# Optimization experiments

Hardware: AMD Instinct MI355X
Metric: run time of the kernel (lower is better)

The kernel has to match this reference:

```python
import jax, jax.numpy as jnp
import numpy as np
from jax import lax

B, CIN, H, W = 8, 3, 256, 256
CMID = 16          # conv out channels == config.in_channels
DM = 256           # d_model
P = 2              # patch size (hardcoded in Downsample)
DI = 512           # d_inner = expand * d_model
NH, HD, NS, KC = 8, 64, 128, 4   # heads, headdim, d_state, d_conv
CONVDIM = DI + 2 * NS            # 768
PROJ = 2 * DI + 2 * NS + NH      # 1288


def _sincos2d(dim, gs):
    # 2d sin-cos positional embedding, matches get_2d_sincos_pos_embed
    def emb1d(d, pos):
        omega = 1.0 / (10000.0 ** (jnp.arange(d // 2, dtype=jnp.float32) / (d / 2.0)))
        out = pos[:, None] * omega[None, :]
        return jnp.concatenate([jnp.sin(out), jnp.cos(out)], axis=1)
    g = jnp.arange(gs, dtype=jnp.float32)
    grid = jnp.stack(jnp.meshgrid(g, g), 0).reshape(2, -1)  # [2, gs*gs]
    return jnp.concatenate([emb1d(dim // 2, grid[0]), emb1d(dim // 2, grid[1])], 1)


def _mamba2(u, in_proj_w, conv1d_w, conv1d_b, dt_bias, A_log, D, norm_w, out_proj_w):
    b, l, _ = u.shape
    zxbcdt = jnp.einsum('bld,pd->blp', u, in_proj_w)              # [b,l,1288]
    z = zxbcdt[..., :DI]
    xBC = zxbcdt[..., DI:DI + CONVDIM]
    dt = zxbcdt[..., DI + CONVDIM:]                                # [b,l,NH]
    # causal depthwise conv1d over sequence, then SiLU
    xc = lax.conv_general_dilated(xBC.transpose(0, 2, 1), conv1d_w, (1,), [(KC - 1, 0)],
                                  feature_group_count=CONVDIM,
                                  dimension_numbers=('NCH', 'OIH', 'NCH'))
    xBC = jax.nn.silu(xc + conv1d_b[None, :, None]).transpose(0, 2, 1)
    xh = xBC[..., :DI].reshape(b, l, NH, HD)                       # [b,l,h,p]
    Bm = xBC[..., DI:DI + NS]                                      # [b,l,n]
    Cm = xBC[..., DI + NS:]                                        # [b,l,n]
    dt = jax.nn.softplus(dt + dt_bias)                             # [b,l,h]
    dA = jnp.exp(dt * (-jnp.exp(A_log)))                           # [b,l,h]
    dtx = dt[..., None] * xh                                       # [b,l,h,p]

    def step(s, inp):
        dtx_t, B_t, C_t, dA_t = inp
        s = s * dA_t[..., None, None] + dtx_t[..., None] * B_t[:, None, None, :]
        return s, jnp.einsum('bhpn,bn->bhp', s, C_t)

    s0 = jnp.zeros((b, NH, HD, NS), u.dtype)
    _, ys = lax.scan(step, s0, (dtx.transpose(1, 0, 2, 3), Bm.transpose(1, 0, 2),
                                Cm.transpose(1, 0, 2), dA.transpose(1, 0, 2)))
    y = ys.transpose(1, 0, 2, 3) + D[None, None, :, None] * xh     # [b,l,h,p]
    y = y.reshape(b, l, DI) * jax.nn.silu(z)                       # gated
    y = y * lax.rsqrt(jnp.mean(y * y, -1, keepdims=True) + 1e-5) * norm_w
    return jnp.einsum('bld,od->blo', y, out_proj_w)


def setup_inputs() -> dict:
    key = jax.random.key(0)
    ks = jax.random.split(key, 12)
    r = lambda i, s, sc: jax.random.normal(ks[i], s, jnp.float32) * sc
    return {
        'x': jax.random.normal(ks[0], (B, CIN, H, W), jnp.float32),
        'conv_w': r(1, (CMID, CIN, 3, 3), 0.1), 'conv_b': jnp.zeros((CMID,), jnp.float32),
        'bn_gamma': jnp.ones((CMID,), jnp.float32), 'bn_beta': jnp.zeros((CMID,), jnp.float32),
        'patch_w': r(2, (DM, CMID, P, P), 0.1), 'patch_b': jnp.zeros((DM,), jnp.float32),
        'in_proj_w': r(3, (PROJ, DM), 0.02),
        'conv1d_w': r(4, (CONVDIM, 1, KC), 0.1), 'conv1d_b': jnp.zeros((CONVDIM,), jnp.float32),
        'dt_bias': r(5, (NH,), 0.5),
        'A_log': jax.random.uniform(ks[6], (NH,), jnp.float32),
        'D': jnp.ones((NH,), jnp.float32),
        'norm_w': jnp.ones((DI,), jnp.float32),
        'out_proj_w': r(7, (DM, DI), 0.02),
        'final_w': r(8, (P * P * CMID, DM), 0.02), 'final_b': jnp.zeros((P * P * CMID,), jnp.float32),
    }


def reference(x, conv_w, conv_b, bn_gamma, bn_beta, patch_w, patch_b, in_proj_w,
              conv1d_w, conv1d_b, dt_bias, A_log, D, norm_w, out_proj_w, final_w, final_b):
    # Conv2d k=3 s=2 p=1 -> BatchNorm2d (training-mode batch stats) -> GELU
    h = lax.conv_general_dilated(x, conv_w, (2, 2), [(1, 1), (1, 1)],
                                 dimension_numbers=('NCHW', 'OIHW', 'NCHW')) + conv_b[None, :, None, None]
    mu = jnp.mean(h, (0, 2, 3), keepdims=True)
    var = jnp.var(h, (0, 2, 3), keepdims=True)
    h = (h - mu) * lax.rsqrt(var + 1e-5) * bn_gamma[None, :, None, None] + bn_beta[None, :, None, None]
    h = jax.nn.gelu(h, approximate=False)
    # PatchEmbed: conv k=p s=p, flatten to tokens, add frozen sincos pos embed
    t = lax.conv_general_dilated(h, patch_w, (P, P), 'VALID',
                                 dimension_numbers=('NCHW', 'OIHW', 'NCHW')) + patch_b[None, :, None, None]
    b, d, gh, gw = t.shape
    tok = t.reshape(b, d, gh * gw).transpose(0, 2, 1) + _sincos2d(DM, gh)[None]
    # MambaBlock: Mamba2(x) + x  (layers=1; repo loop discards all but last layer)
    y = _mamba2(tok, in_proj_w, conv1d_w, conv1d_b, dt_bias, A_log, D, norm_w, out_proj_w) + tok
    # FinalLayer: linear only (norm_final is unused in its forward)
    o = jnp.einsum('bld,od->blo', y, final_w) + final_b
    # unpatchify
    o = o.reshape(b, gh, gw, P, P, CMID)
    o = jnp.einsum('nhwpqc->nchpwq', o).reshape(b, CMID, gh * P, gw * P)
    return o
```

## Files before the change

kernel.cpp:

```cpp
#include <hip/hip_runtime.h>
#include <math.h>

#define B_  8
#define CIN 3
#define HIN 256
#define WIN 256
#define CMID 16
#define HMID 128
#define WMID 128
#define DM 256
#define L_ 4096
#define DI 512
#define NH 8
#define HD 64
#define NS 128
#define KC 4
#define CONVDIM 768
#define PROJ 1288
#define NPADIN 1408
#define MTOK (B_*L_)
#define QCH 128
#define NCH 32

typedef unsigned short bf16;
typedef __attribute__((ext_vector_type(8))) short bf16x8;
typedef __attribute__((ext_vector_type(4))) float f32x4;

__device__ inline float bf2f(bf16 u) { return __uint_as_float(((unsigned int)u) << 16); }
__device__ inline bf16 f2bf(float f) {
  unsigned int x = __float_as_uint(f);
  return (bf16)((x + 0x7fffu + ((x >> 16) & 1u)) >> 16);
}
__device__ inline unsigned int pack2bf(float a, float b) {
  return (unsigned int)f2bf(a) | ((unsigned int)f2bf(b) << 16);
}

__global__ void k_conv1(const float* __restrict__ x, const float* __restrict__ w,
                        const float* __restrict__ bias, float* __restrict__ out) {
  int idx = blockIdx.x*256 + threadIdx.x;
  if (idx >= B_*CMID*HMID*WMID) return;
  int xo = idx & 127, yo = (idx>>7)&127, co = (idx>>14)&15, b = idx>>18;
  float acc = bias[co];
  const float* xb = x + (size_t)b*CIN*HIN*WIN;
  const float* wc = w + co*CIN*9;
  #pragma unroll
  for (int ci=0; ci<CIN; ci++)
    #pragma unroll
    for (int ky=0; ky<3; ky++) {
      int yi = 2*yo - 1 + ky;
      if (yi < 0 || yi >= HIN) continue;
      #pragma unroll
      for (int kx=0; kx<3; kx++) {
        int xi = 2*xo - 1 + kx;
        if (xi < 0 || xi >= WIN) continue;
        acc += xb[(ci*HIN + yi)*WIN + xi] * wc[(ci*3+ky)*3+kx];
      }
    }
  out[idx] = acc;
}

__global__ __launch_bounds__(256) void k_bnstatsA(const float* __restrict__ h, float2* __restrict__ part) {
  int blk = blockIdx.x;
  const float4* base = (const float4*)(h + ((size_t)(blk>>2))*16384 + (blk&3)*4096);
  int tid = threadIdx.x;
  float s=0.f, s2=0.f;
  #pragma unroll
  for (int i=0;i<4;i++){
    float4 v = base[i*256 + tid];
    s += v.x+v.y+v.z+v.w;
    s2 += v.x*v.x + v.y*v.y + v.z*v.z + v.w*v.w;
  }
  #pragma unroll
  for (int off=1; off<64; off<<=1) { s += __shfl_xor(s, off); s2 += __shfl_xor(s2, off); }
  __shared__ float sb[2][4];
  if ((tid&63)==0){ sb[0][tid>>6]=s; sb[1][tid>>6]=s2; }
  __syncthreads();
  if (tid==0) part[blk] = make_float2(sb[0][0]+sb[0][1]+sb[0][2]+sb[0][3],
                                      sb[1][0]+sb[1][1]+sb[1][2]+sb[1][3]);
}

__global__ void k_bnstatsB(const float2* __restrict__ part, float* __restrict__ stats) {
  int lane = threadIdx.x;
  int c = lane >> 2, j0 = lane & 3;
  float s=0.f, s2=0.f;
  #pragma unroll
  for (int j=j0; j<32; j+=4){
    int b = j >> 2, chunk = j & 3;
    float2 p = part[(b*16+c)*4 + chunk];
    s += p.x; s2 += p.y;
  }
  s += __shfl_xor(s,1); s2 += __shfl_xor(s2,1);
  s += __shfl_xor(s,2); s2 += __shfl_xor(s2,2);
  if (j0==0){
    const float inv = 1.f/131072.f;
    float mean = s*inv;
    float var  = s2*inv - mean*mean;
    stats[c]      = mean;
    stats[16 + c] = rsqrtf(var + 1e-5f);
  }
}

__global__ __launch_bounds__(256) void k_patch(const float* __restrict__ h, const float* __restrict__ pw,
                       const float* __restrict__ pb, const float* __restrict__ stats,
                       const float* __restrict__ gamma, const float* __restrict__ beta,
                       bf16* __restrict__ tok) {
  int grp = blockIdx.x;
  int b = grp >> 9, g8 = grp & 511;
  int g0 = g8 << 3;
  int gy = g0 >> 6, gx0 = g0 & 63;
  __shared__ float sh[8][64];
  int tid = threadIdx.x;
  {
    int tk = tid >> 5, jj = (tid & 31)*2;
    int ci = jj >> 2, p = (jj >> 1) & 1;
    const float* src = &h[((size_t)(b*CMID+ci)*HMID + 2*gy+p)*WMID + 2*(gx0+tk)];
    float2 xv = *(const float2*)src;
    float mean = stats[ci], rstd = stats[16+ci];
    float sc = rstd*gamma[ci], be = beta[ci] - mean*sc;
    float v0 = xv.x*sc + be;
    float v1 = xv.y*sc + be;
    v0 = 0.5f*v0*(1.f + erff(v0*0.70710678118654752f));
    v1 = 0.5f*v1*(1.f + erff(v1*0.70710678118654752f));
    sh[tk][jj] = v0; sh[tk][jj+1] = v1;
  }
  __syncthreads();
  int d = tid;
  float wr[64];
  #pragma unroll
  for (int i4=0;i4<16;i4++) *(float4*)&wr[i4*4] = *(const float4*)&pw[d*64 + i4*4];
  float bias = pb[d];
  int i = d & 63;
  float omega = expf(-(float)i * (9.210340371976184f/64.f));
  #pragma unroll
  for (int tk=0;tk<8;tk++){
    float acc = bias;
    #pragma unroll
    for (int j=0;j<64;j++) acc = fmaf(sh[tk][j], wr[j], acc);
    float gv = (d < 128) ? (float)(gx0+tk) : (float)gy;
    float ph = gv * omega;
    float pos = (d & 64) ? __cosf(ph) : __sinf(ph);
    tok[((size_t)((b<<12) + g0 + tk))*DM + d] = f2bf(acc + pos);
  }
}

__global__ void k_cvtw(const float* __restrict__ src, bf16* __restrict__ dst,
                       int N, int kshift, int total) {
  int idx = blockIdx.x*256 + threadIdx.x;
  if (idx >= total) return;
  int n = idx >> kshift;
  dst[idx] = (n < N) ? f2bf(src[idx]) : (bf16)0;
}

template<int EPI>
__global__ __launch_bounds__(256) void k_mgemm(
    const bf16* __restrict__ A, const bf16* __restrict__ Bw, int K,
    bf16* __restrict__ o_z, bf16* __restrict__ o_x,
    bf16* __restrict__ o_y, const bf16* __restrict__ res,
    const float* __restrict__ dt_bias, const float* __restrict__ A_log,
    float* __restrict__ dtv, float* __restrict__ dAv,
    float* __restrict__ o_f, const float* __restrict__ fbias) {
  __shared__ __align__(16) bf16 sA[2][128*32];
  __shared__ __align__(16) bf16 sB[2][128*32];
  int tid = threadIdx.x;
  int lane = tid & 63, wid = tid >> 6;
  int wr = wid >> 1, wc = wid & 1;
  int m0 = blockIdx.x*128, n0 = blockIdx.y*128;
  int nk = K >> 5;
  f32x4 acc[4][4];
  #pragma unroll
  for (int i=0;i<4;i++)
    #pragma unroll
    for (int j=0;j<4;j++)
      acc[i][j] = (f32x4){0.f,0.f,0.f,0.f};

  auto stage = [&](int buf, int ks){
    int kk = ks << 5;
    #pragma unroll
    for (int i=0;i<2;i++){
      int j = i*256 + tid;
      int row = j >> 2, cc = j & 3;
      int kg = cc ^ (row & 3);
      unsigned ldsoff = (unsigned)((i*256 + wid*64) * 16);
      __builtin_amdgcn_global_load_lds(
        (const __attribute__((address_space(1))) void*)(A + (size_t)(m0+row)*K + kk + kg*8),
        (__attribute__((address_space(3))) void*)((char*)&sA[buf][0] + ldsoff), 16, 0, 0);
      __builtin_amdgcn_global_load_lds(
        (const __attribute__((address_space(1))) void*)(Bw + (size_t)(n0+row)*K + kk + kg*8),
        (__attribute__((address_space(3))) void*)((char*)&sB[buf][0] + ldsoff), 16, 0, 0);
    }
  };

  int r = lane & 15, q = lane >> 4;
  int kgo = (q ^ (r & 3)) << 3;

  stage(0, 0);
  for (int ks=0; ks<nk; ++ks){
    int cur = ks & 1;
    __syncthreads();
    if (ks+1 < nk) stage(cur^1, ks+1);
    bf16x8 af[4], bfv[4];
    #pragma unroll
    for (int mf=0;mf<4;mf++){
      int rowm = wr*64 + mf*16 + r;
      af[mf] = *(const bf16x8*)&sA[cur][rowm*32 + kgo];
    }
    #pragma unroll
    for (int nf=0;nf<4;nf++){
      int rown = wc*64 + nf*16 + r;
      bfv[nf] = *(const bf16x8*)&sB[cur][rown*32 + kgo];
    }
    #pragma unroll
    for (int mf=0;mf<4;mf++)
      #pragma unroll
      for (int nf=0;nf<4;nf++)
        acc[mf][nf] = __builtin_amdgcn_mfma_f32_16x16x32_bf16(af[mf], bfv[nf], acc[mf][nf], 0, 0, 0);
  }

  #pragma unroll
  for (int mf=0;mf<4;mf++){
    #pragma unroll
    for (int nf=0;nf<4;nf++){
      int n = n0 + wc*64 + nf*16 + r;
      int mbase = m0 + wr*64 + mf*16 + q*4;
      #pragma unroll
      for (int rr=0;rr<4;rr++){
        int m = mbase + rr;
        float val = acc[mf][nf][rr];
        if (EPI == 0){
          if (n < DI) {
            o_z[(size_t)m*DI + n] = f2bf(val);
          } else if (n < DI + CONVDIM) {
            o_x[(size_t)m*CONVDIM + (n - DI)] = f2bf(val);
          } else if (n < PROJ) {
            int hh = n - (DI + CONVDIM);
            float xv = val + dt_bias[hh];
            float dt = (xv > 20.f) ? xv : log1pf(expf(xv));
            dtv[(size_t)m*NH + hh] = dt;
            dAv[(size_t)m*NH + hh] = expf(-expf(A_log[hh]) * dt);
          }
        } else if (EPI == 1) {
          o_y[(size_t)m*DM + n] = f2bf(val + bf2f(res[(size_t)m*DM + n]));
        } else {
          if (n < 64) {
            float vv = val + fbias[n];
            int b = m >> 12, g = m & 4095;
            int gy = g >> 6, gx = g & 63;
            int p = n >> 5, qq = (n>>4)&1, cc2 = n & 15;
            o_f[(((size_t)(b*CMID+cc2))*HMID + 2*gy+p)*WMID + (2*gx+qq)] = vv;
          }
        }
      }
    }
  }
}

__global__ __launch_bounds__(256) void k_conv1d(const bf16* __restrict__ xpre, const float* __restrict__ cw,
                         const float* __restrict__ cb, bf16* __restrict__ xbc) {
  int idx = blockIdx.x*256 + threadIdx.x;
  int gch = idx % 96;
  int tb  = idx / 96;
  int ch0 = gch*8;
  int bl0 = tb*8;
  int l0 = bl0 & (L_-1);
  float wv[32];
  #pragma unroll
  for (int i=0;i<8;i++) *(float4*)&wv[i*4] = *(const float4*)&cw[ch0*KC + i*4];
  float bs[8];
  *(float4*)&bs[0] = *(const float4*)&cb[ch0];
  *(float4*)&bs[4] = *(const float4*)&cb[ch0+4];
  uint4 rows[11];
  #pragma unroll
  for (int j=0;j<11;j++){
    int lk = l0 - 3 + j;
    if (lk < 0) rows[j] = make_uint4(0u,0u,0u,0u);
    else rows[j] = *(const uint4*)(xpre + ((size_t)bl0 - 3 + j)*CONVDIM + ch0);
  }
  #pragma unroll
  for (int t=0;t<8;t++){
    float acc[8];
    #pragma unroll
    for (int i=0;i<8;i++) acc[i] = bs[i];
    #pragma unroll
    for (int k=0;k<KC;k++){
      uint4 u = rows[t+k];
      unsigned uu[4]={u.x,u.y,u.z,u.w};
      #pragma unroll
      for (int c2=0;c2<4;c2++){
        float lo = __uint_as_float(uu[c2]<<16);
        float hi = __uint_as_float(uu[c2]&0xffff0000u);
        acc[c2*2]   = fmaf(wv[(c2*2)*4 + k],   lo, acc[c2*2]);
        acc[c2*2+1] = fmaf(wv[(c2*2+1)*4 + k], hi, acc[c2*2+1]);
      }
    }
    unsigned ou[4];
    #pragma unroll
    for (int c2=0;c2<4;c2++){
      float v0 = acc[c2*2], v1 = acc[c2*2+1];
      v0 = v0 / (1.f + __expf(-v0));
      v1 = v1 / (1.f + __expf(-v1));
      ou[c2] = pack2bf(v0, v1);
    }
    *(uint4*)(xbc + (size_t)(bl0+t)*CONVDIM + ch0) = make_uint4(ou[0],ou[1],ou[2],ou[3]);
  }
}

__global__ __launch_bounds__(256) void k_ssd1(const bf16* __restrict__ xbc,
    const float* __restrict__ dtv, const float* __restrict__ A_log,
    bf16* __restrict__ ys, bf16* __restrict__ Sst) {
  int blk = blockIdx.x;
  int c = blk & (NCH-1), h = (blk>>5)&7, b = blk>>8;
  int tid = threadIdx.x;
  int lane = tid & 63, wid = tid >> 6;
  int r = lane & 15, q = lane >> 4;
  size_t rowbase = (size_t)b*L_ + (size_t)c*QCH;
  float eA = __expf(A_log[h]);

  __shared__ __align__(16) bf16 sB[128*128];
  __shared__ __align__(16) bf16 sC[128*128];
  __shared__ __align__(16) bf16 sDX[64*128];
  __shared__ __align__(16) bf16 sBT[128*128];
  __shared__ float sDT[128];
  __shared__ float sL[128];
  __shared__ float sWS[128];
  __shared__ float sWT[2];

  #pragma unroll
  for (int i=0;i<16;i++){
    int id = i*256 + tid;
    int row = id >> 5, cg = id & 31;
    uint4 u = *(const uint4*)(xbc + (rowbase+row)*CONVDIM + DI + cg*8);
    if (cg < 16) *(uint4*)&sB[row*128 + ((cg ^ (row&15))<<3)] = u;
    else { int cg2 = cg-16; *(uint4*)&sC[row*128 + ((cg2 ^ (row&15))<<3)] = u; }
  }
  if (tid < 128) sDT[tid] = dtv[(rowbase+tid)*NH + h];
  __syncthreads();

  float inc = 0.f;
  if (tid < 128){
    inc = sDT[tid];
    #pragma unroll
    for (int off=1; off<64; off<<=1){
      float u = __shfl_up(inc, off);
      if (lane >= off) inc += u;
    }
    if (lane==63) sWT[wid] = inc;
  }
  __syncthreads();
  if (tid < 128){
    if (wid==1) inc += sWT[0];
    sL[tid] = inc;
  }
  {
    int s = tid >> 1, ph = tid & 1;
    float dts = sDT[s];
    const bf16* xs = xbc + (rowbase+s)*CONVDIM + h*HD + ph*32;
    #pragma unroll
    for (int i8=0;i8<4;i8++){
      ushort4 u0 = *(const ushort4*)(xs + i8*8);
      ushort4 u1 = *(const ushort4*)(xs + i8*8 + 4);
      unsigned short uu[8] = {u0.x,u0.y,u0.z,u0.w,u1.x,u1.y,u1.z,u1.w};
      #pragma unroll
      for (int j=0;j<8;j++){
        int p = ph*32 + i8*8 + j;
        sDX[p*128 + (((s>>3) ^ (p&15))<<3) + (s&7)] = f2bf(dts * bf2f(uu[j]));
      }
    }
  }
  __syncthreads();

  int wr = wid >> 1, wc = wid & 1;
  f32x4 accG[4][4];
  #pragma unroll
  for (int i=0;i<4;i++)
    #pragma unroll
    for (int j=0;j<4;j++) accG[i][j] = (f32x4){0.f,0.f,0.f,0.f};
  #pragma unroll
  for (int ks=0; ks<4; ks++){
    bf16x8 af[4], bfv[4];
    #pragma unroll
    for (int mf=0;mf<4;mf++){
      int t = wr*64 + mf*16 + r;
      af[mf] = *(const bf16x8*)&sC[t*128 + (((ks*4+q) ^ (t&15))<<3)];
    }
    #pragma unroll
    for (int nf=0;nf<4;nf++){
      int s = wc*64 + nf*16 + r;
      bfv[nf] = *(const bf16x8*)&sB[s*128 + (((ks*4+q) ^ (s&15))<<3)];
    }
    #pragma unroll
    for (int mf=0;mf<4;mf++)
      #pragma unroll
      for (int nf=0;nf<4;nf++)
        accG[mf][nf] = __builtin_amdgcn_mfma_f32_16x16x32_bf16(af[mf], bfv[nf], accG[mf][nf], 0, 0, 0);
  }
  __syncthreads();

  bf16* sW = sC;
  #pragma unroll
  for (int mf=0;mf<4;mf++){
    #pragma unroll
    for (int nf=0;nf<4;nf++){
      int s = wc*64 + nf*16 + r;
      float Ls = sL[s];
      #pragma unroll
      for (int rr=0;rr<4;rr++){
        int t = wr*64 + mf*16 + q*4 + rr;
        float wvv = 0.f;
        if (s <= t) wvv = accG[mf][nf][rr] * __expf(-eA*(sL[t]-Ls));
        sW[t*128 + (((s>>3) ^ (t&15))<<3) + (s&7)] = f2bf(wvv);
      }
    }
  }
  if (tid < 128) sWS[tid] = __expf(-eA*(sL[127]-sL[tid]));
  __syncthreads();

  {
    int n = tid >> 1, ph = tid & 1;
    #pragma unroll
    for (int i8=0;i8<8;i8++){
      unsigned short vals[8];
      #pragma unroll
      for (int j=0;j<8;j++){
        int s = ph*64 + i8*8 + j;
        float bv = bf2f(sB[s*128 + (((n>>3) ^ (s&15))<<3) + (n&7)]);
        vals[j] = f2bf(bv * sWS[s]);
      }
      int s8 = ph*8 + i8;
      *(uint4*)&sBT[n*128 + ((s8 ^ (n&15))<<3)] = *(const uint4*)vals;
    }
  }
  __syncthreads();

  {
    int wr2 = wid >> 1, wc2 = wid & 1;
    f32x4 accY[4][2];
    #pragma unroll
    for (int i=0;i<4;i++){ accY[i][0]=(f32x4){0.f,0.f,0.f,0.f}; accY[i][1]=(f32x4){0.f,0.f,0.f,0.f}; }
    #pragma unroll
    for (int ks=0; ks<4; ks++){
      bf16x8 af[4], bfv[2];
      #pragma unroll
      for (int mf=0;mf<4;mf++){
        int t = wr2*64 + mf*16 + r;
        af[mf] = *(const bf16x8*)&sW[t*128 + (((ks*4+q) ^ (t&15))<<3)];
      }
      #pragma unroll
      for (int nf=0;nf<2;nf++){
        int p = wc2*32 + nf*16 + r;
        bfv[nf] = *(const bf16x8*)&sDX[p*128 + (((ks*4+q) ^ (p&15))<<3)];
      }
      #pragma unroll
      for (int mf=0;mf<4;mf++)
        #pragma unroll
        for (int nf=0;nf<2;nf++)
          accY[mf][nf] = __builtin_amdgcn_mfma_f32_16x16x32_bf16(af[mf], bfv[nf], accY[mf][nf], 0, 0, 0);
    }
    #pragma unroll
    for (int mf=0;mf<4;mf++){
      #pragma unroll
      for (int nf=0;nf<2;nf++){
        int p = wc2*32 + nf*16 + r;
        #pragma unroll
        for (int rr=0;rr<4;rr++){
          int t = wr2*64 + mf*16 + q*4 + rr;
          ys[(rowbase+t)*DI + h*HD + p] = f2bf(accY[mf][nf][rr]);
        }
      }
    }
  }

  {
    int wrp = wid >> 1, wcn = wid & 1;
    f32x4 accT[2][4];
    #pragma unroll
    for (int i=0;i<2;i++)
      #pragma unroll
      for (int j=0;j<4;j++) accT[i][j] = (f32x4){0.f,0.f,0.f,0.f};
    #pragma unroll
    for (int ks=0; ks<4; ks++){
      bf16x8 af[2], bfv[4];
      #pragma unroll
      for (int mf=0;mf<2;mf++){
        int p = wrp*32 + mf*16 + r;
        af[mf] = *(const bf16x8*)&sDX[p*128 + (((ks*4+q) ^ (p&15))<<3)];
      }
      #pragma unroll
      for (int nf=0;nf<4;nf++){
        int n = wcn*64 + nf*16 + r;
        bfv[nf] = *(const bf16x8*)&sBT[n*128 + (((ks*4+q) ^ (n&15))<<3)];
      }
      #pragma unroll
      for (int mf=0;mf<2;mf++)
        #pragma unroll
        for (int nf=0;nf<4;nf++)
          accT[mf][nf] = __builtin_amdgcn_mfma_f32_16x16x32_bf16(af[mf], bfv[nf], accT[mf][nf], 0, 0, 0);
    }
    size_t sb = (((size_t)(b*NH+h))*NCH + c)*8192;
    #pragma unroll
    for (int mf=0;mf<2;mf++){
      #pragma unroll
      for (int nf=0;nf<4;nf++){
        int n = wcn*64 + nf*16 + r;
        #pragma unroll
        for (int rr=0;rr<4;rr++){
          int p = wrp*32 + mf*16 + q*4 + rr;
          Sst[sb + (size_t)p*128 + n] = f2bf(accT[mf][nf][rr]);
        }
      }
    }
  }
}

template<int NCHT, int QCHT>
__global__ __launch_bounds__(256) void k_scan2(bf16* __restrict__ Sst, const float* __restrict__ dAv) {
  constexpr int SEG = QCHT/16;
  int blk = blockIdx.x;
  int bh = blk>>2, q = blk&3;
  int b = bh>>3, h = bh&7;
  int tid = threadIdx.x;
  __shared__ float sP[NCHT];
  {
    int c = tid / SEG, seg = tid & (SEG-1);
    float prod = 1.f;
    size_t base = ((size_t)b*L_ + c*QCHT + seg*16)*NH + h;
    #pragma unroll
    for (int k=0;k<16;k++) prod *= dAv[base + (size_t)k*NH];
    #pragma unroll
    for (int off=1; off<SEG; off<<=1) prod *= __shfl_xor(prod, off);
    if (seg==0) sP[c] = prod;
  }
  __syncthreads();
  int e0 = q*2048 + tid*8;
  float acc[8];
  #pragma unroll
  for (int j=0;j<8;j++) acc[j]=0.f;
  size_t sbase = (size_t)bh*NCHT*8192 + e0;
  for (int c=0;c<NCHT;c++){
    bf16* ptr = Sst + sbase + (size_t)c*8192;
    uint4 u = *(const uint4*)ptr;
    unsigned int uu[4] = {u.x,u.y,u.z,u.w};
    float tv[8];
    #pragma unroll
    for (int k=0;k<4;k++){
      tv[2*k]   = __uint_as_float(uu[k]<<16);
      tv[2*k+1] = __uint_as_float(uu[k]&0xffff0000u);
    }
    uint4 o;
    o.x = pack2bf(acc[0],acc[1]); o.y = pack2bf(acc[2],acc[3]);
    o.z = pack2bf(acc[4],acc[5]); o.w = pack2bf(acc[6],acc[7]);
    asm volatile("s_waitcnt vmcnt(0)" ::: "memory");
    *(uint4*)ptr = o;
    float P = sP[c];
    #pragma unroll
    for (int j=0;j<8;j++) acc[j] = tv[j] + P*acc[j];
  }
}

__global__ __launch_bounds__(256) void k_ssd3(const bf16* __restrict__ xbc,
    const float* __restrict__ dtv, const float* __restrict__ A_log,
    const bf16* __restrict__ Sst, bf16* __restrict__ ys) {
  int blk = blockIdx.x;
  int c = blk & (NCH-1), h = (blk>>5)&7, b = blk>>8;
  int tid = threadIdx.x;
  int lane = tid & 63, wid = tid >> 6;
  int r = lane & 15, q = lane >> 4;
  size_t rowbase = (size_t)b*L_ + (size_t)c*QCH;
  float eA = __expf(A_log[h]);

  __shared__ __align__(16) bf16 sC[128*128];
  __shared__ float sDT[128];
  __shared__ float sL[128];
  __shared__ float sAt[128];
  __shared__ float sWT[2];

  #pragma unroll
  for (int i=0;i<8;i++){
    int id = i*256 + tid;
    int row = id >> 4, cg = id & 15;
    uint4 u = *(const uint4*)(xbc + (rowbase+row)*CONVDIM + DI + NS + cg*8);
    *(uint4*)&sC[row*128 + ((cg ^ (row&15))<<3)] = u;
  }
  if (tid < 128) sDT[tid] = dtv[(rowbase+tid)*NH + h];
  __syncthreads();
  float inc = 0.f;
  if (tid < 128){
    inc = sDT[tid];
    #pragma unroll
    for (int off=1; off<64; off<<=1){
      float u = __shfl_up(inc, off);
      if (lane >= off) inc += u;
    }
    if (lane==63) sWT[wid] = inc;
  }
  __syncthreads();
  if (tid < 128){
    if (wid==1) inc += sWT[0];
    sL[tid] = inc;
    sAt[tid] = __expf(-eA*inc);
  }
  __syncthreads();

  int wr2 = wid >> 1, wc2 = wid & 1;
  size_t sb = (((size_t)(b*NH+h))*NCH + c)*8192;
  f32x4 accP[4][2];
  #pragma unroll
  for (int i=0;i<4;i++){ accP[i][0]=(f32x4){0.f,0.f,0.f,0.f}; accP[i][1]=(f32x4){0.f,0.f,0.f,0.f}; }
  #pragma unroll
  for (int ks=0; ks<4; ks++){
    bf16x8 af[4], bfv[2];
    #pragma unroll
    for (int mf=0;mf<4;mf++){
      int t = wr2*64 + mf*16 + r;
      af[mf] = *(const bf16x8*)&sC[t*128 + (((ks*4+q) ^ (t&15))<<3)];
    }
    #pragma unroll
    for (int nf=0;nf<2;nf++){
      int p = wc2*32 + nf*16 + r;
      bfv[nf] = *(const bf16x8*)(Sst + sb + (size_t)p*128 + ks*32 + q*8);
    }
    #pragma unroll
    for (int mf=0;mf<4;mf++)
      #pragma unroll
      for (int nf=0;nf<2;nf++)
        accP[mf][nf] = __builtin_amdgcn_mfma_f32_16x16x32_bf16(af[mf], bfv[nf], accP[mf][nf], 0, 0, 0);
  }
  #pragma unroll
  for (int mf=0;mf<4;mf++){
    #pragma unroll
    for (int nf=0;nf<2;nf++){
      int p = wc2*32 + nf*16 + r;
      #pragma unroll
      for (int rr=0;rr<4;rr++){
        int t = wr2*64 + mf*16 + q*4 + rr;
        bf16* yp = ys + (rowbase+t)*DI + h*HD + p;
        *yp = f2bf(bf2f(*yp) + sAt[t]*accP[mf][nf][rr]);
      }
    }
  }
}

__global__ __launch_bounds__(256) void k_combine(bf16* __restrict__ ys, const bf16* __restrict__ xbc,
                         const bf16* __restrict__ z, const float* __restrict__ Dp,
                         const float* __restrict__ nw) {
  int bl = blockIdx.x;
  int tid = threadIdx.x;
  bf16* yrow = ys + (size_t)bl*DI;
  const bf16* xrow = xbc + (size_t)bl*CONVDIM;
  const bf16* zrow = z + (size_t)bl*DI;
  float v[2]; float ss = 0.f;
  #pragma unroll
  for (int i=0;i<2;i++) {
    int d = tid + i*256;
    float xh = bf2f(xrow[d]);
    float y = bf2f(yrow[d]) + Dp[d>>6]*xh;
    float zv = bf2f(zrow[d]);
    y *= zv / (1.f + expf(-zv));
    v[i] = y; ss += y*y;
  }
  #pragma unroll
  for (int off=1; off<64; off<<=1) ss += __shfl_xor(ss, off);
  __shared__ float sb[4];
  if ((tid&63)==0) sb[tid>>6]=ss;
  __syncthreads();
  float total = sb[0]+sb[1]+sb[2]+sb[3];
  float scale = rsqrtf(total * (1.f/512.f) + 1e-5f);
  #pragma unroll
  for (int i=0;i<2;i++) {
    int d = tid + i*256;
    yrow[d] = f2bf(v[i]*scale*nw[d]);
  }
}

extern "C" void kernel_launch(void* const* d_in, const int* in_sizes, int n_in,
                              void* d_out, int out_size, void* d_ws, size_t ws_size,
                              hipStream_t stream) {
  const float* x         = (const float*)d_in[0];
  const float* conv_w    = (const float*)d_in[1];
  const float* conv_b    = (const float*)d_in[2];
  const float* bn_gamma  = (const float*)d_in[3];
  const float* bn_beta   = (const float*)d_in[4];
  const float* patch_w   = (const float*)d_in[5];
  const float* patch_b   = (const float*)d_in[6];
  const float* in_proj_w = (const float*)d_in[7];
  const float* conv1d_w  = (const float*)d_in[8];
  const float* conv1d_b  = (const float*)d_in[9];
  const float* dt_bias   = (const float*)d_in[10];
  const float* A_log     = (const float*)d_in[11];
  const float* Dp        = (const float*)d_in[12];
  const float* norm_w    = (const float*)d_in[13];
  const float* out_proj_w= (const float*)d_in[14];
  const float* final_w   = (const float*)d_in[15];
  const float* final_b   = (const float*)d_in[16];
  float* out = (float*)d_out;

  char* Wb = (char*)d_ws;
  float* h_buf = (float*)(Wb + 0);
  bf16*  winb  = (bf16*)(Wb + 0);
  bf16*  woutb = (bf16*)(Wb + 0);
  bf16*  wfinb = (bf16*)(Wb + 262144);
  bf16*  xpost = (bf16*)(Wb + 0);
  float2* part = (float2*)(Wb + 50331648);
  bf16*  tok   = (bf16*)(Wb + 50331648);
  bf16*  zbuf  = (bf16*)(Wb + 67108864);
  bf16*  y2b   = (bf16*)(Wb + 67108864);
  bf16*  xpre  = (bf16*)(Wb + 100663296);
  bf16*  ysb   = (bf16*)(Wb + 100663296);
  bf16*  Sst   = (bf16*)(Wb + 134217728);
  float* dtv   = (float*)(Wb + 134217728 + 33554432);
  float* dAv   = dtv + 262144;
  float* stats = dAv + 262144;
  const size_t NEED = 134217728ull + 33554432 + 2097152 + 256;
  if (ws_size < NEED) {
    hipMemsetAsync(d_out, 0, (size_t)out_size*sizeof(float), stream);
    return;
  }

  k_conv1<<<dim3((B_*CMID*HMID*WMID)/256), dim3(256), 0, stream>>>(x, conv_w, conv_b, h_buf);
  k_bnstatsA<<<dim3(512), dim3(256), 0, stream>>>(h_buf, part);
  k_bnstatsB<<<dim3(1), dim3(64), 0, stream>>>(part, stats);
  k_patch<<<dim3(MTOK/8), dim3(256), 0, stream>>>(h_buf, patch_w, patch_b, stats, bn_gamma, bn_beta, tok);
  k_cvtw<<<dim3((NPADIN*DM)/256), dim3(256), 0, stream>>>(in_proj_w, winb, PROJ, 8, NPADIN*DM);
  k_mgemm<0><<<dim3(MTOK/128, NPADIN/128), dim3(256), 0, stream>>>(tok, winb, DM,
      zbuf, xpre, nullptr, nullptr, dt_bias, A_log, dtv, dAv, nullptr, nullptr);
  k_conv1d<<<dim3((MTOK/8*96)/256), dim3(256), 0, stream>>>(xpre, conv1d_w, conv1d_b, xpost);
  k_ssd1<<<dim3(B_*NH*NCH), dim3(256), 0, stream>>>(xpost, dtv, A_log, ysb, Sst);
  k_scan2<NCH,QCH><<<dim3(B_*NH*4), dim3(256), 0, stream>>>(Sst, dAv);
  k_ssd3<<<dim3(B_*NH*NCH), dim3(256), 0, stream>>>(xpost, dtv, A_log, Sst, ysb);
  k_combine<<<dim3(MTOK), dim3(256), 0, stream>>>(ysb, xpost, zbuf, Dp, norm_w);
  k_cvtw<<<dim3((DM*DI)/256), dim3(256), 0, stream>>>(out_proj_w, woutb, DM, 9, DM*DI);
  k_cvtw<<<dim3((128*DM)/256), dim3(256), 0, stream>>>(final_w, wfinb, 64, 8, 128*DM);
  k_mgemm<1><<<dim3(MTOK/128, DM/128), dim3(256), 0, stream>>>(ysb, woutb, DI,
      nullptr, nullptr, y2b, tok, nullptr, nullptr, nullptr, nullptr, nullptr, nullptr);
  k_mgemm<2><<<dim3(MTOK/128, 1), dim3(256), 0, stream>>>(y2b, wfinb, DM,
      nullptr, nullptr, nullptr, nullptr, nullptr, nullptr, nullptr, nullptr, out, final_b);
}
```

Baseline: 383.8 us.

## Restructure SSD chunk kernel to 512 threads with transposed MFMA tiles and vector stores

k_ssd1 now runs 512 threads per block. Each GEMM is re-tiled so results land with contiguous output dimensions, which lets the ys and state stores be packed uint2 writes instead of scalar bf16 stores. The dt scaling moves out of the x staging into the decay weights (W and the B-transpose), so x is loaded raw with 16-byte loads and one barrier goes away. k_ssd3 is transposed in the same way to get vectorized read-modify-write of ys. The cost is more threads per block competing for the same large shared-memory footprint, and a changed rounding point for dt, since it is now applied in the weights rather than on x before the bf16 conversion.

Result: faster. 363.4 us (-5.3%).

```diff
diff --git a/kernel.cpp b/kernel.cpp
--- a/kernel.cpp
+++ b/kernel.cpp
@@ -304,7 +304,7 @@
   }
 }
 
-__global__ __launch_bounds__(256) void k_ssd1(const bf16* __restrict__ xbc,
+__global__ __launch_bounds__(512) void k_ssd1(const bf16* __restrict__ xbc,
     const float* __restrict__ dtv, const float* __restrict__ A_log,
     bf16* __restrict__ ys, bf16* __restrict__ Sst) {
   int blk = blockIdx.x;
@@ -325,13 +325,31 @@
   __shared__ float sWT[2];
 
   #pragma unroll
-  for (int i=0;i<16;i++){
-    int id = i*256 + tid;
+  for (int i=0;i<8;i++){
+    int id = i*512 + tid;
     int row = id >> 5, cg = id & 31;
     uint4 u = *(const uint4*)(xbc + (rowbase+row)*CONVDIM + DI + cg*8);
     if (cg < 16) *(uint4*)&sB[row*128 + ((cg ^ (row&15))<<3)] = u;
     else { int cg2 = cg-16; *(uint4*)&sC[row*128 + ((cg2 ^ (row&15))<<3)] = u; }
   }
+  {
+    int s0 = (tid >> 3)*2;
+    int p0 = (tid & 7)*8;
+    const bf16* x0 = xbc + (rowbase+s0)*CONVDIM + h*HD + p0;
+    uint4 u0 = *(const uint4*)x0;
+    uint4 u1 = *(const uint4*)(x0 + CONVDIM);
+    unsigned a0[4]={u0.x,u0.y,u0.z,u0.w}, a1[4]={u1.x,u1.y,u1.z,u1.w};
+    int cb2 = s0 >> 3, se = s0 & 7;
+    #pragma unroll
+    for (int jp=0;jp<4;jp++){
+      unsigned w0=a0[jp], w1=a1[jp];
+      unsigned lo = (w0 & 0xffffu) | (w1 << 16);
+      unsigned hi = (w0 >> 16) | (w1 & 0xffff0000u);
+      int pA = p0 + jp*2, pB = pA+1;
+      *(unsigned*)&sDX[pA*128 + ((cb2 ^ (pA&15))<<3) + se] = lo;
+      *(unsigned*)&sDX[pB*128 + ((cb2 ^ (pB&15))<<3) + se] = hi;
+    }
+  }
   if (tid < 128) sDT[tid] = dtv[(rowbase+tid)*NH + h];
   __syncthreads();
 
@@ -350,45 +368,28 @@
     if (wid==1) inc += sWT[0];
     sL[tid] = inc;
   }
-  {
-    int s = tid >> 1, ph = tid & 1;
-    float dts = sDT[s];
-    const bf16* xs = xbc + (rowbase+s)*CONVDIM + h*HD + ph*32;
-    #pragma unroll
-    for (int i8=0;i8<4;i8++){
-      ushort4 u0 = *(const ushort4*)(xs + i8*8);
-      ushort4 u1 = *(const ushort4*)(xs + i8*8 + 4);
-      unsigned short uu[8] = {u0.x,u0.y,u0.z,u0.w,u1.x,u1.y,u1.z,u1.w};
-      #pragma unroll
-      for (int j=0;j<8;j++){
-        int p = ph*32 + i8*8 + j;
-        sDX[p*128 + (((s>>3) ^ (p&15))<<3) + (s&7)] = f2bf(dts * bf2f(uu[j]));
-      }
-    }
-  }
-  __syncthreads();
 
   int wr = wid >> 1, wc = wid & 1;
-  f32x4 accG[4][4];
-  #pragma unroll
-  for (int i=0;i<4;i++)
+  f32x4 accG[2][4];
+  #pragma unroll
+  for (int i=0;i<2;i++)
     #pragma unroll
     for (int j=0;j<4;j++) accG[i][j] = (f32x4){0.f,0.f,0.f,0.f};
   #pragma unroll
   for (int ks=0; ks<4; ks++){
-    bf16x8 af[4], bfv[4];
-    #pragma unroll
-    for (int mf=0;mf<4;mf++){
-      int t = wr*64 + mf*16 + r;
-      af[mf] = *(const bf16x8*)&sC[t*128 + (((ks*4+q) ^ (t&15))<<3)];
+    bf16x8 af[2], bfv[4];
+    #pragma unroll
+    for (int mf=0;mf<2;mf++){
+      int s = wr*32 + mf*16 + r;
+      af[mf] = *(const bf16x8*)&sB[s*128 + (((ks*4+q) ^ (s&15))<<3)];
     }
     #pragma unroll
     for (int nf=0;nf<4;nf++){
-      int s = wc*64 + nf*16 + r;
-      bfv[nf] = *(const bf16x8*)&sB[s*128 + (((ks*4+q) ^ (s&15))<<3)];
-    }
-    #pragma unroll
-    for (int mf=0;mf<4;mf++)
+      int t = wc*64 + nf*16 + r;
+      bfv[nf] = *(const bf16x8*)&sC[t*128 + (((ks*4+q) ^ (t&15))<<3)];
+    }
+    #pragma unroll
+    for (int mf=0;mf<2;mf++)
       #pragma unroll
       for (int nf=0;nf<4;nf++)
         accG[mf][nf] = __builtin_amdgcn_mfma_f32_16x16x32_bf16(af[mf], bfv[nf], accG[mf][nf], 0, 0, 0);
@@ -397,115 +398,116 @@
 
   bf16* sW = sC;
   #pragma unroll
-  for (int mf=0;mf<4;mf++){
+  for (int mf=0;mf<2;mf++){
+    int sb4 = wr*32 + mf*16 + q*4;
+    int cb4 = sb4 >> 3, se4 = sb4 & 7;
     #pragma unroll
     for (int nf=0;nf<4;nf++){
-      int s = wc*64 + nf*16 + r;
-      float Ls = sL[s];
+      int t = wc*64 + nf*16 + r;
+      float Lt = sL[t];
+      float w[4];
       #pragma unroll
       for (int rr=0;rr<4;rr++){
-        int t = wr*64 + mf*16 + q*4 + rr;
-        float wvv = 0.f;
-        if (s <= t) wvv = accG[mf][nf][rr] * __expf(-eA*(sL[t]-Ls));
-        sW[t*128 + (((s>>3) ^ (t&15))<<3) + (s&7)] = f2bf(wvv);
-      }
-    }
-  }
-  if (tid < 128) sWS[tid] = __expf(-eA*(sL[127]-sL[tid]));
+        int s = sb4 + rr;
+        float v = 0.f;
+        if (s <= t) v = accG[mf][nf][rr] * sDT[s] * __expf(-eA*(Lt - sL[s]));
+        w[rr] = v;
+      }
+      *(uint2*)&sW[t*128 + ((cb4 ^ (t&15))<<3) + se4] =
+          make_uint2(pack2bf(w[0],w[1]), pack2bf(w[2],w[3]));
+    }
+  }
+  if (tid < 128) sWS[tid] = sDT[tid]*__expf(-eA*(sL[127]-sL[tid]));
   __syncthreads();
 
   {
-    int n = tid >> 1, ph = tid & 1;
-    #pragma unroll
-    for (int i8=0;i8<8;i8++){
+    int n = tid >> 2, sg = tid & 3;
+    #pragma unroll
+    for (int i8=0;i8<4;i8++){
       unsigned short vals[8];
       #pragma unroll
       for (int j=0;j<8;j++){
-        int s = ph*64 + i8*8 + j;
+        int s = sg*32 + i8*8 + j;
         float bv = bf2f(sB[s*128 + (((n>>3) ^ (s&15))<<3) + (n&7)]);
         vals[j] = f2bf(bv * sWS[s]);
       }
-      int s8 = ph*8 + i8;
+      int s8 = sg*4 + i8;
       *(uint4*)&sBT[n*128 + ((s8 ^ (n&15))<<3)] = *(const uint4*)vals;
     }
   }
   __syncthreads();
 
   {
-    int wr2 = wid >> 1, wc2 = wid & 1;
-    f32x4 accY[4][2];
-    #pragma unroll
-    for (int i=0;i<4;i++){ accY[i][0]=(f32x4){0.f,0.f,0.f,0.f}; accY[i][1]=(f32x4){0.f,0.f,0.f,0.f}; }
+    int wrp = wid >> 2, wct = wid & 3;
+    f32x4 acc2[2][2];
+    #pragma unroll
+    for (int i=0;i<2;i++){ acc2[i][0]=(f32x4){0.f,0.f,0.f,0.f}; acc2[i][1]=(f32x4){0.f,0.f,0.f,0.f}; }
     #pragma unroll
     for (int ks=0; ks<4; ks++){
-      bf16x8 af[4], bfv[2];
-      #pragma unroll
-      for (int mf=0;mf<4;mf++){
-        int t = wr2*64 + mf*16 + r;
-        af[mf] = *(const bf16x8*)&sW[t*128 + (((ks*4+q) ^ (t&15))<<3)];
-      }
-      #pragma unroll
-      for (int nf=0;nf<2;nf++){
-        int p = wc2*32 + nf*16 + r;
-        bfv[nf] = *(const bf16x8*)&sDX[p*128 + (((ks*4+q) ^ (p&15))<<3)];
-      }
-      #pragma unroll
-      for (int mf=0;mf<4;mf++)
-        #pragma unroll
-        for (int nf=0;nf<2;nf++)
-          accY[mf][nf] = __builtin_amdgcn_mfma_f32_16x16x32_bf16(af[mf], bfv[nf], accY[mf][nf], 0, 0, 0);
-    }
-    #pragma unroll
-    for (int mf=0;mf<4;mf++){
-      #pragma unroll
-      for (int nf=0;nf<2;nf++){
-        int p = wc2*32 + nf*16 + r;
-        #pragma unroll
-        for (int rr=0;rr<4;rr++){
-          int t = wr2*64 + mf*16 + q*4 + rr;
-          ys[(rowbase+t)*DI + h*HD + p] = f2bf(accY[mf][nf][rr]);
-        }
-      }
-    }
-  }
-
-  {
-    int wrp = wid >> 1, wcn = wid & 1;
-    f32x4 accT[2][4];
-    #pragma unroll
-    for (int i=0;i<2;i++)
-      #pragma unroll
-      for (int j=0;j<4;j++) accT[i][j] = (f32x4){0.f,0.f,0.f,0.f};
-    #pragma unroll
-    for (int ks=0; ks<4; ks++){
-      bf16x8 af[2], bfv[4];
+      bf16x8 af[2], bfv[2];
       #pragma unroll
       for (int mf=0;mf<2;mf++){
         int p = wrp*32 + mf*16 + r;
         af[mf] = *(const bf16x8*)&sDX[p*128 + (((ks*4+q) ^ (p&15))<<3)];
       }
       #pragma unroll
-      for (int nf=0;nf<4;nf++){
-        int n = wcn*64 + nf*16 + r;
-        bfv[nf] = *(const bf16x8*)&sBT[n*128 + (((ks*4+q) ^ (n&15))<<3)];
+      for (int nf=0;nf<2;nf++){
+        int t = wct*32 + nf*16 + r;
+        bfv[nf] = *(const bf16x8*)&sW[t*128 + (((ks*4+q) ^ (t&15))<<3)];
       }
       #pragma unroll
       for (int mf=0;mf<2;mf++)
         #pragma unroll
-        for (int nf=0;nf<4;nf++)
-          accT[mf][nf] = __builtin_amdgcn_mfma_f32_16x16x32_bf16(af[mf], bfv[nf], accT[mf][nf], 0, 0, 0);
+        for (int nf=0;nf<2;nf++)
+          acc2[mf][nf] = __builtin_amdgcn_mfma_f32_16x16x32_bf16(af[mf], bfv[nf], acc2[mf][nf], 0, 0, 0);
+    }
+    #pragma unroll
+    for (int mf=0;mf<2;mf++){
+      int pb = wrp*32 + mf*16 + q*4;
+      #pragma unroll
+      for (int nf=0;nf<2;nf++){
+        int t = wct*32 + nf*16 + r;
+        f32x4 v = acc2[mf][nf];
+        *(uint2*)(ys + (rowbase+t)*DI + h*HD + pb) =
+            make_uint2(pack2bf(v[0],v[1]), pack2bf(v[2],v[3]));
+      }
+    }
+  }
+
+  {
+    int wrn = wid >> 1, wcp = wid & 1;
+    f32x4 acc3[2][2];
+    #pragma unroll
+    for (int i=0;i<2;i++){ acc3[i][0]=(f32x4){0.f,0.f,0.f,0.f}; acc3[i][1]=(f32x4){0.f,0.f,0.f,0.f}; }
+    #pragma unroll
+    for (int ks=0; ks<4; ks++){
+      bf16x8 af[2], bfv[2];
+      #pragma unroll
+      for (int mf=0;mf<2;mf++){
+        int n = wrn*32 + mf*16 + r;
+        af[mf] = *(const bf16x8*)&sBT[n*128 + (((ks*4+q) ^ (n&15))<<3)];
+      }
+      #pragma unroll
+      for (int nf=0;nf<2;nf++){
+        int p = wcp*32 + nf*16 + r;
+        bfv[nf] = *(const bf16x8*)&sDX[p*128 + (((ks*4+q) ^ (p&15))<<3)];
+      }
+      #pragma unroll
+      for (int mf=0;mf<2;mf++)
+        #pragma unroll
+        for (int nf=0;nf<2;nf++)
+          acc3[mf][nf] = __builtin_amdgcn_mfma_f32_16x16x32_bf16(af[mf], bfv[nf], acc3[mf][nf], 0, 0, 0);
     }
     size_t sb = (((size_t)(b*NH+h))*NCH + c)*8192;
     #pragma unroll
     for (int mf=0;mf<2;mf++){
-      #pragma unroll
-      for (int nf=0;nf<4;nf++){
-        int n = wcn*64 + nf*16 + r;
-        #pragma unroll
-        for (int rr=0;rr<4;rr++){
-          int p = wrp*32 + mf*16 + q*4 + rr;
-          Sst[sb + (size_t)p*128 + n] = f2bf(accT[mf][nf][rr]);
-        }
+      int nb = wrn*32 + mf*16 + q*4;
+      #pragma unroll
+      for (int nf=0;nf<2;nf++){
+        int p = wcp*32 + nf*16 + r;
+        f32x4 v = acc3[mf][nf];
+        *(uint2*)(Sst + sb + (size_t)p*128 + nb) =
+            make_uint2(pack2bf(v[0],v[1]), pack2bf(v[2],v[3]));
       }
     }
   }
@@ -569,7 +571,6 @@
 
   __shared__ __align__(16) bf16 sC[128*128];
   __shared__ float sDT[128];
-  __shared__ float sL[128];
   __shared__ float sAt[128];
   __shared__ float sWT[2];
 
@@ -595,46 +596,50 @@
   __syncthreads();
   if (tid < 128){
     if (wid==1) inc += sWT[0];
-    sL[tid] = inc;
     sAt[tid] = __expf(-eA*inc);
   }
   __syncthreads();
 
-  int wr2 = wid >> 1, wc2 = wid & 1;
+  int wrp = wid >> 1, wct = wid & 1;
   size_t sb = (((size_t)(b*NH+h))*NCH + c)*8192;
-  f32x4 accP[4][2];
-  #pragma unroll
-  for (int i=0;i<4;i++){ accP[i][0]=(f32x4){0.f,0.f,0.f,0.f}; accP[i][1]=(f32x4){0.f,0.f,0.f,0.f}; }
+  f32x4 accP[2][4];
+  #pragma unroll
+  for (int i=0;i<2;i++)
+    #pragma unroll
+    for (int j=0;j<4;j++) accP[i][j] = (f32x4){0.f,0.f,0.f,0.f};
   #pragma unroll
   for (int ks=0; ks<4; ks++){
-    bf16x8 af[4], bfv[2];
-    #pragma unroll
-    for (int mf=0;mf<4;mf++){
-      int t = wr2*64 + mf*16 + r;
-      af[mf] = *(const bf16x8*)&sC[t*128 + (((ks*4+q) ^ (t&15))<<3)];
-    }
-    #pragma unroll
-    for (int nf=0;nf<2;nf++){
-      int p = wc2*32 + nf*16 + r;
-      bfv[nf] = *(const bf16x8*)(Sst + sb + (size_t)p*128 + ks*32 + q*8);
-    }
-    #pragma unroll
-    for (int mf=0;mf<4;mf++)
-      #pragma unroll
-      for (int nf=0;nf<2;nf++)
+    bf16x8 af[2], bfv[4];
+    #pragma unroll
+    for (int mf=0;mf<2;mf++){
+      int p = wrp*32 + mf*16 + r;
+      af[mf] = *(const bf16x8*)(Sst + sb + (size_t)p*128 + ks*32 + q*8);
+    }
+    #pragma unroll
+    for (int nf=0;nf<4;nf++){
+      int t = wct*64 + nf*16 + r;
+      bfv[nf] = *(const bf16x8*)&sC[t*128 + (((ks*4+q) ^ (t&15))<<3)];
+    }
+    #pragma unroll
+    for (int mf=0;mf<2;mf++)
+      #pragma unroll
+      for (int nf=0;nf<4;nf++)
         accP[mf][nf] = __builtin_amdgcn_mfma_f32_16x16x32_bf16(af[mf], bfv[nf], accP[mf][nf], 0, 0, 0);
   }
   #pragma unroll
-  for (int mf=0;mf<4;mf++){
-    #pragma unroll
-    for (int nf=0;nf<2;nf++){
-      int p = wc2*32 + nf*16 + r;
-      #pragma unroll
-      for (int rr=0;rr<4;rr++){
-        int t = wr2*64 + mf*16 + q*4 + rr;
-        bf16* yp = ys + (rowbase+t)*DI + h*HD + p;
-        *yp = f2bf(bf2f(*yp) + sAt[t]*accP[mf][nf][rr]);
-      }
+  for (int mf=0;mf<2;mf++){
+    int pb = wrp*32 + mf*16 + q*4;
+    #pragma unroll
+    for (int nf=0;nf<4;nf++){
+      int t = wct*64 + nf*16 + r;
+      float at = sAt[t];
+      bf16* yp = ys + (rowbase+t)*DI + h*HD + pb;
+      uint2 old = *(uint2*)yp;
+      float o0 = bf2f((bf16)(old.x & 0xffffu))  + at*accP[mf][nf][0];
+      float o1 = bf2f((bf16)(old.x >> 16))      + at*accP[mf][nf][1];
+      float o2 = bf2f((bf16)(old.y & 0xffffu))  + at*accP[mf][nf][2];
+      float o3 = bf2f((bf16)(old.y >> 16))      + at*accP[mf][nf][3];
+      *(uint2*)yp = make_uint2(pack2bf(o0,o1), pack2bf(o2,o3));
     }
   }
 }
@@ -723,7 +728,7 @@
   k_mgemm<0><<<dim3(MTOK/128, NPADIN/128), dim3(256), 0, stream>>>(tok, winb, DM,
       zbuf, xpre, nullptr, nullptr, dt_bias, A_log, dtv, dAv, nullptr, nullptr);
   k_conv1d<<<dim3((MTOK/8*96)/256), dim3(256), 0, stream>>>(xpre, conv1d_w, conv1d_b, xpost);
-  k_ssd1<<<dim3(B_*NH*NCH), dim3(256), 0, stream>>>(xpost, dtv, A_log, ysb, Sst);
+  k_ssd1<<<dim3(B_*NH*NCH), dim3(512), 0, stream>>>(xpost, dtv, A_log, ysb, Sst);
   k_scan2<NCH,QCH><<<dim3(B_*NH*4), dim3(256), 0, stream>>>(Sst, dAv);
   k_ssd3<<<dim3(B_*NH*NCH), dim3(256), 0, stream>>>(xpost, dtv, A_log, Sst, ysb);
   k_combine<<<dim3(MTOK), dim3(256), 0, stream>>>(ysb, xpost, zbuf, Dp, norm_w);
```
